# Optimization experiments

Hardware: AMD Instinct MI355X
Metric: run time of the kernel (lower is better)

## Reference

```python
import jax, jax.numpy as jnp
import numpy as np

NUM_QUBITS = 15
DEPTH = 3
BATCH = 512
DIM = 2 ** NUM_QUBITS


def _apply_1q_batched(state, gate, q, n):
    # state: [B, 2^n] complex64, gate: [B, 2, 2] complex64, qubit q (little-endian)
    B = state.shape[0]
    L, R = 2 ** (n - 1 - q), 2 ** q
    s = state.reshape(B, L, 2, R)
    return jnp.einsum('bij,bljr->blir', gate, s).reshape(B, -1)


def _apply_1q_shared(state, gate, q, n):
    # gate: [2, 2] shared across batch
    B = state.shape[0]
    L, R = 2 ** (n - 1 - q), 2 ** q
    s = state.reshape(B, L, 2, R)
    return jnp.einsum('ij,bljr->blir', gate, s).reshape(B, -1)


def _apply_cz(state, q, n):
    # CZ on adjacent qubits (q, q+1): sign flip on |..11..>
    B = state.shape[0]
    L, R = 2 ** (n - 2 - q), 2 ** q
    s = state.reshape(B, L, 2, 2, R)
    phase = jnp.array([[1.0, 1.0], [1.0, -1.0]], dtype=state.dtype)
    return (s * phase[None, None, :, :, None]).reshape(B, -1)


def _simulate(state_batch, theta, n, depth):
    B = state_batch.shape[0]
    cdtype = jnp.complex64
    state = jnp.zeros((B, 2 ** n), dtype=cdtype).at[:, 0].set(1.0)
    # RX encoding layer: per-sample angles x_q on wire q
    for q in range(n):
        half = 0.5 * state_batch[:, q]
        c = jnp.cos(half).astype(cdtype)
        s = jnp.sin(half).astype(cdtype)
        gate = jnp.stack([jnp.stack([c, -1j * s], axis=-1),
                          jnp.stack([-1j * s, c], axis=-1)], axis=-2)  # [B,2,2]
        state = _apply_1q_batched(state, gate, q, n)
    # Variational layers: RY(theta) per wire, then CZ chain
    idx = 0
    for _ in range(depth):
        for q in range(n):
            half = 0.5 * theta[idx]
            idx += 1
            c = jnp.cos(half).astype(cdtype)
            s = jnp.sin(half).astype(cdtype)
            gate = jnp.stack([jnp.stack([c, -s]), jnp.stack([s, c])])  # [2,2]
            state = _apply_1q_shared(state, gate, q, n)
        for q in range(n - 1):
            state = _apply_cz(state, q, n)
    return state


def _z_signs(n):
    # signs[k, q] = +1 if bit q of basis index k is 0 else -1
    idx = jnp.arange(2 ** n, dtype=jnp.int32)
    bits = (idx[:, None] >> jnp.arange(n, dtype=jnp.int32)[None, :]) & 1
    return (1.0 - 2.0 * bits).astype(jnp.float32)  # [2^n, n]


def setup_inputs() -> dict:
    key = jax.random.key(0)
    k1, k2, k3, k4 = jax.random.split(key, 4)
    state_batch = jax.random.normal(k1, (BATCH, NUM_QUBITS), dtype=jnp.float32)
    theta = jax.random.normal(k2, (NUM_QUBITS * DEPTH,), dtype=jnp.float32)
    bound = 1.0 / np.sqrt(NUM_QUBITS)
    head_w = jax.random.uniform(k3, (1, NUM_QUBITS), jnp.float32, -bound, bound)
    head_b = jax.random.uniform(k4, (1,), jnp.float32, -bound, bound)
    return {"state_batch": state_batch, "theta": theta, "head_w": head_w, "head_b": head_b}


def reference(state_batch, theta, head_w, head_b):
    n = NUM_QUBITS
    state = _simulate(state_batch, theta, n, DEPTH)  # [B, 2^n] complex64
    probs = state.real ** 2 + state.imag ** 2        # [B, 2^n] float32
    zq = probs @ _z_signs(n)                         # [B, n], col q = <Z_q>
    # qiskit Pauli string 'I'*j + 'Z' + ...: output col j is Z on qubit n-1-j
    expect = zq[:, ::-1]
    out = expect @ head_w.T + head_b                 # [B, 1]
    return out.squeeze(-1)
```

## Files before the change

kernel.cpp:

```cpp
#include <hip/hip_runtime.h>

#define NQ 15

template<int T>
__device__ inline void apply_ry(float (&re)[32], float (&im)[32], float cg, float sg) {
#pragma unroll
    for (int x = 0; x < 32; x++) {
        if (!(x & (1 << T))) {
            const int y = x | (1 << T);
            float r0 = re[x], i0 = im[x], r1 = re[y], i1 = im[y];
            re[x] = cg * r0 - sg * r1;
            im[x] = cg * i0 - sg * i1;
            re[y] = sg * r0 + cg * r1;
            im[y] = sg * i0 + cg * i1;
        }
    }
}

template<int T, int U>
__device__ inline void apply_cz(float (&re)[32], float (&im)[32]) {
#pragma unroll
    for (int x = 0; x < 32; x++) {
        if (((x >> T) & 1) && ((x >> U) & 1)) { re[x] = -re[x]; im[x] = -im[x]; }
    }
}

__global__ __launch_bounds__(256)
void HybridRegression_lightcone_kernel(const float* __restrict__ sb,
                                       const float* __restrict__ theta,
                                       const float* __restrict__ hw,
                                       const float* __restrict__ hb,
                                       float* __restrict__ out,
                                       int batch) {
    const int wave = threadIdx.x >> 6;
    const int lane = threadIdx.x & 63;
    const int b = blockIdx.x * 4 + wave;

    float contrib = 0.0f;

    if (b < batch && lane < NQ) {
        const int q = lane;

        float pc[5], ps[5];
#pragma unroll
        for (int w = 0; w < 5; w++) {
            const int j = q - 2 + w;
            const float a = (j >= 0 && j < NQ) ? sb[b * NQ + j] : 0.0f;
            const float h = 0.5f * a;
            pc[w] = cosf(h);
            ps[w] = sinf(h);
        }

        float re[32], im[32];
        re[0] = 1.0f; im[0] = 0.0f;
#pragma unroll
        for (int w = 0; w < 5; w++) {
#pragma unroll
            for (int x = 0; x < 16; x++) {
                if (x < (1 << w)) {
                    const int y = x + (1 << w);
                    re[y] =  im[x] * ps[w];
                    im[y] = -re[x] * ps[w];
                    re[x] *= pc[w];
                    im[x] *= pc[w];
                }
            }
        }

        float c1[5], s1[5];
#pragma unroll
        for (int w = 0; w < 5; w++) {
            const int j = q - 2 + w;
            const float th = (j >= 0 && j < NQ) ? theta[0 * NQ + j] : 0.0f;
            c1[w] = cosf(0.5f * th);
            s1[w] = sinf(0.5f * th);
        }
        float c2[3], s2[3];
#pragma unroll
        for (int w = 0; w < 3; w++) {
            const int j = q - 1 + w;
            const float th = (j >= 0 && j < NQ) ? theta[1 * NQ + j] : 0.0f;
            c2[w] = cosf(0.5f * th);
            s2[w] = sinf(0.5f * th);
        }
        const float th3 = theta[2 * NQ + q];
        const float c3 = cosf(0.5f * th3), s3 = sinf(0.5f * th3);

        apply_ry<0>(re, im, c1[0], s1[0]);
        apply_ry<1>(re, im, c1[1], s1[1]);
        apply_ry<2>(re, im, c1[2], s1[2]);
        apply_ry<3>(re, im, c1[3], s1[3]);
        apply_ry<4>(re, im, c1[4], s1[4]);
        apply_cz<0, 1>(re, im);
        apply_cz<1, 2>(re, im);
        apply_cz<2, 3>(re, im);
        apply_cz<3, 4>(re, im);

        apply_ry<1>(re, im, c2[0], s2[0]);
        apply_ry<2>(re, im, c2[1], s2[1]);
        apply_ry<3>(re, im, c2[2], s2[2]);
        apply_cz<1, 2>(re, im);
        apply_cz<2, 3>(re, im);

        apply_ry<2>(re, im, c3, s3);

        float zq = 0.0f;
#pragma unroll
        for (int x = 0; x < 32; x++) {
            const float p = re[x] * re[x] + im[x] * im[x];
            zq += (x & 4) ? -p : p;
        }

        contrib = hw[(NQ - 1) - q] * zq;
    }

#pragma unroll
    for (int off = 32; off >= 1; off >>= 1)
        contrib += __shfl_xor(contrib, off, 64);

    if (lane == 0 && b < batch)
        out[b] = contrib + hb[0];
}

extern "C" void kernel_launch(void* const* d_in, const int* in_sizes, int n_in,
                              void* d_out, int out_size, void* d_ws, size_t ws_size,
                              hipStream_t stream) {
    const float* sb    = (const float*)d_in[0];
    const float* theta = (const float*)d_in[1];
    const float* hw    = (const float*)d_in[2];
    const float* hb    = (const float*)d_in[3];
    float* out = (float*)d_out;

    const int batch = in_sizes[0] / NQ;
    const int blocks = (batch + 3) / 4;

    hipLaunchKernelGGL(HybridRegression_lightcone_kernel,
                       dim3(blocks), dim3(256), 0, stream,
                       sb, theta, hw, hb, out, batch);
}
```

Measured before the change: 64.45 us.

## Fold RX·RY into product state, share trig via shuffles, analytic final RY

Each lane now computes its own qubit's sincos once, and neighbouring lanes fetch the values with wave shuffles instead of recomputing redundant trig for a 5-qubit window. The first RX and RY layers are merged into a single per-qubit 2-vector, so the initial 32-amplitude product state is built directly and the five RY applications are skipped. The CZ chains are merged into single parity passes. The last RY on the target qubit is folded into the Z expectation as a closed-form combination of a population difference and a cross term. This cuts ALU and transcendental work per lane, at the cost of more shuffles and a heavier algebraic rewrite to verify.

```diff
diff --git a/kernel.cpp b/kernel.cpp
--- a/kernel.cpp
+++ b/kernel.cpp
@@ -17,108 +17,107 @@
     }
 }
 
-template<int T, int U>
-__device__ inline void apply_cz(float (&re)[32], float (&im)[32]) {
+__global__ __launch_bounds__(256)
+void HybridRegression_lightcone2_kernel(const float* __restrict__ sb,
+                                        const float* __restrict__ theta,
+                                        const float* __restrict__ hw,
+                                        const float* __restrict__ hb,
+                                        float* __restrict__ out,
+                                        int batch) {
+    const int wave = threadIdx.x >> 6;
+    const int lane = threadIdx.x & 63;
+    int b = blockIdx.x * 4 + wave;
+    const bool bv = (b < batch);
+    if (!bv) b = batch - 1;
+
+    const int q = lane;
+    const bool qv = (q < NQ);
+
+    const float a  = qv ? sb[b * NQ + q]    : 0.0f;
+    const float t1 = qv ? theta[q]          : 0.0f;
+    const float t2 = qv ? theta[NQ + q]     : 0.0f;
+    const float t3 = qv ? theta[2 * NQ + q] : 0.0f;
+
+    float sh, ch;  sincosf(0.5f * a,  &sh, &ch);
+    float s1, c1;  sincosf(0.5f * t1, &s1, &c1);
+    float s2, c2;  sincosf(0.5f * t2, &s2, &c2);
+    float s3, c3;  sincosf(t3,        &s3, &c3);
+
+    const float x0 = c1 * ch, y0 = s1 * sh;
+    const float x1 = s1 * ch, y1 = -c1 * sh;
+
+    float fx0[5], fy0[5], fx1[5], fy1[5];
+#pragma unroll
+    for (int w = 0; w < 5; w++) {
+        const int j = q - 2 + w;
+        const int src = (j >= 0 && j < NQ) ? j : NQ;
+        fx0[w] = __shfl(x0, src, 64);
+        fy0[w] = __shfl(y0, src, 64);
+        fx1[w] = __shfl(x1, src, 64);
+        fy1[w] = __shfl(y1, src, 64);
+    }
+    float g2c[3], g2s[3];
+#pragma unroll
+    for (int w = 0; w < 3; w++) {
+        const int j = q - 1 + w;
+        const int src = (j >= 0 && j < NQ) ? j : NQ;
+        g2c[w] = __shfl(c2, src, 64);
+        g2s[w] = __shfl(s2, src, 64);
+    }
+
+    float re[32], im[32];
+    re[0] = fx0[0]; im[0] = fy0[0];
+    re[1] = fx1[0]; im[1] = fy1[0];
+#pragma unroll
+    for (int w = 1; w < 5; w++) {
+#pragma unroll
+        for (int x = 0; x < 16; x++) {
+            if (x < (1 << w)) {
+                const int y = x + (1 << w);
+                const float r = re[x], i = im[x];
+                re[y] = r * fx1[w] - i * fy1[w];
+                im[y] = r * fy1[w] + i * fx1[w];
+                re[x] = r * fx0[w] - i * fy0[w];
+                im[x] = r * fy0[w] + i * fx0[w];
+            }
+        }
+    }
+
 #pragma unroll
     for (int x = 0; x < 32; x++) {
-        if (((x >> T) & 1) && ((x >> U) & 1)) { re[x] = -re[x]; im[x] = -im[x]; }
+        const int p = (((x >> 0) & 3) == 3) + (((x >> 1) & 3) == 3)
+                    + (((x >> 2) & 3) == 3) + (((x >> 3) & 3) == 3);
+        if (p & 1) { re[x] = -re[x]; im[x] = -im[x]; }
     }
-}
 
-__global__ __launch_bounds__(256)
-void HybridRegression_lightcone_kernel(const float* __restrict__ sb,
-                                       const float* __restrict__ theta,
-                                       const float* __restrict__ hw,
-                                       const float* __restrict__ hb,
-                                       float* __restrict__ out,
-                                       int batch) {
-    const int wave = threadIdx.x >> 6;
-    const int lane = threadIdx.x & 63;
-    const int b = blockIdx.x * 4 + wave;
+    apply_ry<1>(re, im, g2c[0], g2s[0]);
+    apply_ry<2>(re, im, g2c[1], g2s[1]);
+    apply_ry<3>(re, im, g2c[2], g2s[2]);
 
-    float contrib = 0.0f;
+#pragma unroll
+    for (int x = 0; x < 32; x++) {
+        const int p = (((x >> 1) & 3) == 3) + (((x >> 2) & 3) == 3);
+        if (p & 1) { re[x] = -re[x]; im[x] = -im[x]; }
+    }
 
-    if (b < batch && lane < NQ) {
-        const int q = lane;
+    float zd = 0.0f, zc = 0.0f;
+#pragma unroll
+    for (int x = 0; x < 32; x++) {
+        if (!(x & 4)) {
+            const int y = x | 4;
+            zd += (re[x] * re[x] + im[x] * im[x]) - (re[y] * re[y] + im[y] * im[y]);
+            zc += re[x] * re[y] + im[x] * im[y];
+        }
+    }
+    const float zq = c3 * zd - 2.0f * s3 * zc;
 
-        float pc[5], ps[5];
-#pragma unroll
-        for (int w = 0; w < 5; w++) {
-            const int j = q - 2 + w;
-            const float a = (j >= 0 && j < NQ) ? sb[b * NQ + j] : 0.0f;
-            const float h = 0.5f * a;
-            pc[w] = cosf(h);
-            ps[w] = sinf(h);
-        }
-
-        float re[32], im[32];
-        re[0] = 1.0f; im[0] = 0.0f;
-#pragma unroll
-        for (int w = 0; w < 5; w++) {
-#pragma unroll
-            for (int x = 0; x < 16; x++) {
-                if (x < (1 << w)) {
-                    const int y = x + (1 << w);
-                    re[y] =  im[x] * ps[w];
-                    im[y] = -re[x] * ps[w];
-                    re[x] *= pc[w];
-                    im[x] *= pc[w];
-                }
-            }
-        }
-
-        float c1[5], s1[5];
-#pragma unroll
-        for (int w = 0; w < 5; w++) {
-            const int j = q - 2 + w;
-            const float th = (j >= 0 && j < NQ) ? theta[0 * NQ + j] : 0.0f;
-            c1[w] = cosf(0.5f * th);
-            s1[w] = sinf(0.5f * th);
-        }
-        float c2[3], s2[3];
-#pragma unroll
-        for (int w = 0; w < 3; w++) {
-            const int j = q - 1 + w;
-            const float th = (j >= 0 && j < NQ) ? theta[1 * NQ + j] : 0.0f;
-            c2[w] = cosf(0.5f * th);
-            s2[w] = sinf(0.5f * th);
-        }
-        const float th3 = theta[2 * NQ + q];
-        const float c3 = cosf(0.5f * th3), s3 = sinf(0.5f * th3);
-
-        apply_ry<0>(re, im, c1[0], s1[0]);
-        apply_ry<1>(re, im, c1[1], s1[1]);
-        apply_ry<2>(re, im, c1[2], s1[2]);
-        apply_ry<3>(re, im, c1[3], s1[3]);
-        apply_ry<4>(re, im, c1[4], s1[4]);
-        apply_cz<0, 1>(re, im);
-        apply_cz<1, 2>(re, im);
-        apply_cz<2, 3>(re, im);
-        apply_cz<3, 4>(re, im);
-
-        apply_ry<1>(re, im, c2[0], s2[0]);
-        apply_ry<2>(re, im, c2[1], s2[1]);
-        apply_ry<3>(re, im, c2[2], s2[2]);
-        apply_cz<1, 2>(re, im);
-        apply_cz<2, 3>(re, im);
-
-        apply_ry<2>(re, im, c3, s3);
-
-        float zq = 0.0f;
-#pragma unroll
-        for (int x = 0; x < 32; x++) {
-            const float p = re[x] * re[x] + im[x] * im[x];
-            zq += (x & 4) ? -p : p;
-        }
-
-        contrib = hw[(NQ - 1) - q] * zq;
-    }
+    float contrib = qv ? hw[(NQ - 1) - q] * zq : 0.0f;
 
 #pragma unroll
     for (int off = 32; off >= 1; off >>= 1)
         contrib += __shfl_xor(contrib, off, 64);
 
-    if (lane == 0 && b < batch)
+    if (lane == 0 && bv)
         out[b] = contrib + hb[0];
 }
 
@@ -134,7 +133,7 @@
     const int batch = in_sizes[0] / NQ;
     const int blocks = (batch + 3) / 4;
 
-    hipLaunchKernelGGL(HybridRegression_lightcone_kernel,
+    hipLaunchKernelGGL(HybridRegression_lightcone2_kernel,
                        dim3(blocks), dim3(256), 0, stream,
                        sb, theta, hw, hb, out, batch);
 }
```

Measured after the change: 61.88 us. 1.04x faster.
